# Optimization experiments

Hardware: AMD Instinct MI355X
Metric: run time of the kernel (lower is better)

## Reference

```python
import jax, jax.numpy as jnp
import numpy as np
from jax import lax

UP = 2          # upsampling factor
K = 3           # conv kernel size
PADDING = K // 2
CLAMP = 256.0   # conv_clamp
ACT_GAIN = float(np.sqrt(2.0))  # lrelu def_gain
LRELU_SLOPE = 0.2
_F1 = np.array([1.0, 3.0, 3.0, 1.0], np.float32)
_F1 = _F1 / _F1.sum()  # upfirdn2d.setup_filter normalizes to sum 1


def setup_inputs() -> dict:
    key = jax.random.key(0)
    k1, k2 = jax.random.split(key)
    x = jax.random.normal(k1, (8, 512, 64, 64), jnp.float32)
    weight = jax.random.normal(k2, (256, 512, K, K), jnp.float32)
    bias = jnp.zeros((256,), jnp.float32)
    return {"x": x, "weight": weight, "bias": bias}


def reference(x, weight, bias):
    O, I, kh, kw = weight.shape
    w = weight * (1.0 / np.sqrt(I * kh * kw))  # weight_gain

    # --- conv2d_resample fast path for up=2, kernel>1 ---
    # base padding px0=px1=py0=py1=PADDING, then up>1 adjustments
    fw = _F1.shape[0]
    p0 = PADDING + (fw + UP - 1) // 2
    p1 = PADDING + (fw - UP) // 2
    p0 -= kw - 1
    p1 -= kw - UP
    pt = max(min(-p0, -p1), 0)
    # torch.conv_transpose2d(x, w.transpose(0,1), stride=UP, padding=pt), no weight flip
    # == input-dilated convolution with spatially flipped kernel, pad (k-1-pt)
    y = lax.conv_general_dilated(
        x, jnp.flip(w, (2, 3)),
        window_strides=(1, 1),
        padding=[(kh - 1 - pt, kh - 1 - pt), (kw - 1 - pt, kw - 1 - pt)],
        lhs_dilation=(UP, UP),
        dimension_numbers=('NCHW', 'OIHW', 'NCHW'))  # [N, O, 2H+k-2, 2W+k-2]

    # upfirdn2d: pad (p0+pt, p1+pt) per side, depthwise FIR, gain = up**2
    f2 = jnp.asarray(np.outer(_F1, _F1) * (UP ** 2), jnp.float32)  # [4,4], symmetric
    fk = jnp.broadcast_to(f2[None, None], (O, 1, fw, fw))
    pad = (p0 + pt, p1 + pt)
    y = lax.conv_general_dilated(
        y, fk, (1, 1), padding=[pad, pad],
        dimension_numbers=('NCHW', 'OIHW', 'NCHW'),
        feature_group_count=O)  # [N, O, 2H, 2W]

    # --- bias_act: bias + lrelu * gain, clamp ---
    y = y + bias[None, :, None, None]
    y = jnp.where(y >= 0, y, LRELU_SLOPE * y) * ACT_GAIN
    y = jnp.clip(y, -CLAMP, CLAMP)
    return y
```

## Files before the change

kernel.cpp:

```cpp
#include <hip/hip_runtime.h>
#include <hip/hip_fp16.h>
#include <cstdint>
#include <cmath>


typedef _Float16 f16;
typedef _Float16 f16x8 __attribute__((ext_vector_type(8)));
typedef _Float16 f16x4 __attribute__((ext_vector_type(4)));
typedef float f32x4 __attribute__((ext_vector_type(4)));

#define GLD16(g, l)                                                            \
  __builtin_amdgcn_global_load_lds(                                            \
      (const __attribute__((address_space(1))) void*)(g),                      \
      (__attribute__((address_space(3))) void*)(l), 16, 0, 0)

static const size_t XP_ELEMS  = (size_t)8 * 66 * 66 * 512;
static const size_t XP_BYTES  = XP_ELEMS * 2;
static const size_t WEFF_ELEMS = (size_t)9 * 1024 * 512;
static const size_t WEFF_BYTES = WEFF_ELEMS * 2;

__global__ __launch_bounds__(256) void pad_transpose(const float* __restrict__ x,
                                                     f16* __restrict__ xp) {
  __shared__ f16 tile[64][68];
  const int b = blockIdx.x;
  const int n = b >> 6, h = b & 63, y = h + 1;
  const int t = threadIdx.x;
  for (int c0 = 0; c0 < 512; c0 += 64) {
    if (c0) __syncthreads();
#pragma unroll
    for (int r = 0; r < 16; ++r) {
      int idx = r * 256 + t;
      int cl = idx >> 6, wpos = idx & 63;
      float v = x[(((size_t)(n * 512 + c0 + cl) * 64 + h) << 6) + wpos];
      tile[wpos][cl] = (f16)v;
    }
    __syncthreads();
#pragma unroll
    for (int q = 0; q < 4; ++q) {
      int st = q * 256 + t;
      int xw = st >> 4, c = (st & 15) << 2;
      f16x4 v = *(const f16x4*)&tile[xw][c];
      *(f16x4*)&xp[((size_t)((n * 66 + y) * 66 + xw + 1) << 9) + c0 + c] = v;
    }
  }
}

__global__ __launch_bounds__(256) void weff_kernel(const float* __restrict__ w,
                                                   f16* __restrict__ weff) {
  const int g = blockIdx.x * 256 + threadIdx.x;
  const int o = g >> 9, c = g & 511;
  const float* wp = w + (size_t)(o * 512 + c) * 9;
  float w9[9];
#pragma unroll
  for (int k = 0; k < 9; ++k) w9[k] = wp[k];
  const float f0 = 0.25f, f1 = 0.75f, f2 = 0.75f, f3 = 0.25f;
  const float G[2][3][3] = {
      {{0.f, f0, f1}, {f1, f2, f3}, {f3, 0.f, 0.f}},
      {{0.f, 0.f, f0}, {f0, f1, f2}, {f2, f3, 0.f}}};
  const float scale = 64.f / sqrtf(512.f * 9.f);
#pragma unroll
  for (int py = 0; py < 2; ++py)
#pragma unroll
    for (int dy = 0; dy < 3; ++dy) {
      float ty[3];
#pragma unroll
      for (int bx = 0; bx < 3; ++bx)
        ty[bx] = w9[bx] * G[py][dy][0] + w9[3 + bx] * G[py][dy][1] +
                 w9[6 + bx] * G[py][dy][2];
#pragma unroll
      for (int px = 0; px < 2; ++px)
#pragma unroll
        for (int dx = 0; dx < 3; ++dx) {
          float v = ty[0] * G[px][dx][0] + ty[1] * G[px][dx][1] +
                    ty[2] * G[px][dx][2];
          int s = dy * 3 + dx;
          int col = (o << 2) | (py << 1) | px;
          weff[((size_t)(s * 1024 + col) << 9) + c] = (f16)(v * scale);
        }
    }
}

__global__ __launch_bounds__(256) void conv_main(const f16* __restrict__ xp,
                                                 const f16* __restrict__ weff,
                                                 const float* __restrict__ bias,
                                                 float* __restrict__ out) {
  __shared__ f16 ldsA[128 * 64];
  __shared__ f16 ldsB[128 * 64];
  const int t = threadIdx.x;
  const int lane = t & 63;
  const int wave = t >> 6;
  const int ntile = blockIdx.x;
  const int mtile = blockIdx.y;
  const int n_img = mtile >> 5;
  const int i0 = (mtile & 31) << 1;
  const int col0 = ntile << 7;

  const int c_swz = ((t & 7) ^ ((t >> 3) & 7)) << 3;
  const f16* srcA[4];
  const f16* srcB[4];
#pragma unroll
  for (int q = 0; q < 4; ++q) {
    int pix = (t >> 3) + (q << 5);
    int il = pix >> 6, j = pix & 63;
    srcA[q] = xp + ((size_t)((n_img * 66 + i0 + il) * 66 + j) << 9) + c_swz;
    srcB[q] = weff + ((size_t)(col0 + (t >> 3) + (q << 5)) << 9) + c_swz;
  }
  f16* dstA = ldsA + t * 8;
  f16* dstB = ldsB + t * 8;

  f32x4 acc[4][4];
#pragma unroll
  for (int m = 0; m < 4; ++m)
#pragma unroll
    for (int n = 0; n < 4; ++n) {
      f32x4 z = {0.f, 0.f, 0.f, 0.f};
      acc[m][n] = z;
    }

  const int lrow = lane & 15;
  const int kgrp = lane >> 4;
  const int rA = (wave >> 1) << 6;
  const int cB = (wave & 1) << 6;

  for (int s = 0; s < 9; ++s) {
    const int offA_s = ((s / 3) * 66 + (s % 3)) << 9;
    const int offB_s = s << 19;
    for (int kc = 0; kc < 8; ++kc) {
      const int offA = offA_s + (kc << 6);
      const int offB = offB_s + (kc << 6);
      __syncthreads();
#pragma unroll
      for (int q = 0; q < 4; ++q) GLD16(srcA[q] + offA, dstA + q * 2048);
#pragma unroll
      for (int q = 0; q < 4; ++q) GLD16(srcB[q] + offB, dstB + q * 2048);
      __syncthreads();
#pragma unroll
      for (int kk = 0; kk < 2; ++kk) {
        const int cs = (((kk << 2) | kgrp) ^ (lrow & 7)) << 3;
        f16x8 a[4], b[4];
#pragma unroll
        for (int m = 0; m < 4; ++m)
          a[m] = *(const f16x8*)&ldsA[((rA + (m << 4) + lrow) << 6) + cs];
#pragma unroll
        for (int n = 0; n < 4; ++n)
          b[n] = *(const f16x8*)&ldsB[((cB + (n << 4) + lrow) << 6) + cs];
#pragma unroll
        for (int m = 0; m < 4; ++m)
#pragma unroll
          for (int n = 0; n < 4; ++n)
            acc[m][n] =
                __builtin_amdgcn_mfma_f32_16x16x32_f16(a[m], b[n], acc[m][n], 0, 0, 0);
      }
    }
  }

  const float inv = 1.0f / 64.0f;
#pragma unroll
  for (int nf = 0; nf < 4; ++nf) {
    const int colL = cB + (nf << 4) + lrow;
    const int oG = (col0 + colL) >> 2;
    const int py = (colL >> 1) & 1, px = colL & 1;
    const float bz = bias[oG];
#pragma unroll
    for (int m = 0; m < 4; ++m) {
#pragma unroll
      for (int r = 0; r < 4; ++r) {
        const int rowL = rA + (m << 4) + (kgrp << 2) + r;
        const int ii = i0 + (rowL >> 6), jj = rowL & 63;
        float v = acc[m][nf][r] * inv + bz;
        v = (v < 0.f ? 0.2f * v : v) * 1.41421356237f;
        v = fminf(fmaxf(v, -256.f), 256.f);
        out[((size_t)((n_img * 256 + oG) * 128 + (ii << 1) + py) << 7) +
            (jj << 1) + px] = v;
      }
    }
  }
}

__global__ void naive_conv(const float* __restrict__ x, const float* __restrict__ w,
                           const float* __restrict__ bias, float* __restrict__ out) {
  size_t g = (size_t)blockIdx.x * 256 + threadIdx.x;
  const int xo = g & 127, yo = (int)((g >> 7) & 127);
  const int o = (int)((g >> 14) & 255), n = (int)(g >> 22);
  const int px = xo & 1, py = yo & 1, j = xo >> 1, i = yo >> 1;
  const float f0 = 0.25f, f1 = 0.75f, f2 = 0.75f, f3 = 0.25f;
  const float G0[3][3] = {{0.f, f0, f1}, {f1, f2, f3}, {f3, 0.f, 0.f}};
  const float G1[3][3] = {{0.f, 0.f, f0}, {f0, f1, f2}, {f2, f3, 0.f}};
  const float(*Gy)[3] = py ? G1 : G0;
  const float(*Gx)[3] = px ? G1 : G0;
  float acc = 0.f;
  for (int c = 0; c < 512; ++c) {
    const float* wp = w + ((size_t)o * 512 + c) * 9;
    float w9[9];
#pragma unroll
    for (int k = 0; k < 9; ++k) w9[k] = wp[k];
    float ty[3][3];
#pragma unroll
    for (int dy = 0; dy < 3; ++dy)
#pragma unroll
      for (int bx = 0; bx < 3; ++bx)
        ty[dy][bx] = w9[bx] * Gy[dy][0] + w9[3 + bx] * Gy[dy][1] + w9[6 + bx] * Gy[dy][2];
#pragma unroll
    for (int dy = 0; dy < 3; ++dy) {
      int yy = i + dy - 1;
      if (yy < 0 || yy > 63) continue;
#pragma unroll
      for (int dx = 0; dx < 3; ++dx) {
        int xx = j + dx - 1;
        if (xx < 0 || xx > 63) continue;
        float eff = ty[dy][0] * Gx[dx][0] + ty[dy][1] * Gx[dx][1] + ty[dy][2] * Gx[dx][2];
        acc += x[(((size_t)(n * 512 + c) * 64 + yy) << 6) + xx] * eff;
      }
    }
  }
  float v = acc * (1.f / sqrtf(512.f * 9.f)) + bias[o];
  v = (v < 0.f ? 0.2f * v : v) * 1.41421356237f;
  v = fminf(fmaxf(v, -256.f), 256.f);
  out[g] = v;
}

extern "C" void kernel_launch(void* const* d_in, const int* in_sizes, int n_in,
                              void* d_out, int out_size, void* d_ws, size_t ws_size,
                              hipStream_t stream) {
  const float* x = (const float*)d_in[0];
  const float* w = (const float*)d_in[1];
  const float* bias = (const float*)d_in[2];
  float* out = (float*)d_out;

  const size_t NEED = XP_BYTES + WEFF_BYTES;
  if (ws_size < NEED) {
    naive_conv<<<131072, 256, 0, stream>>>(x, w, bias, out);
    return;
  }
  f16* xp = (f16*)d_ws;
  f16* weff = (f16*)((char*)d_ws + XP_BYTES);

  hipMemsetAsync(d_ws, 0, XP_BYTES, stream);
  pad_transpose<<<512, 256, 0, stream>>>(x, xp);
  weff_kernel<<<512, 256, 0, stream>>>(w, weff);
  conv_main<<<dim3(8, 256), 256, 0, stream>>>(xp, weff, bias, out);
}
```

Before: 553.2 us.

## Rewrite conv GEMM as 256x256 double-buffered pipelined tile with XCD-aware mapping

The main implicit-GEMM kernel moves from a 128x128 tile with 256 threads and single-buffered LDS to a 256x256 tile with 512 threads. LDS is double-buffered and loads are interleaved with MFMA quarter-steps under explicit vmcnt waits, barriers and setprio. Blocks are remapped so tiles that share data land on the same XCD. The full memset of the padded input is replaced by a kernel that zeroes only the border ring, and pad_transpose now runs as more blocks with wider 16-byte stores. The larger tile raises register and LDS pressure, and the hand-tuned barrier schedule is fragile.

```diff
diff --git a/kernel.cpp b/kernel.cpp
--- a/kernel.cpp
+++ b/kernel.cpp
@@ -6,7 +6,6 @@
 
 typedef _Float16 f16;
 typedef _Float16 f16x8 __attribute__((ext_vector_type(8)));
-typedef _Float16 f16x4 __attribute__((ext_vector_type(4)));
 typedef float f32x4 __attribute__((ext_vector_type(4)));
 
 #define GLD16(g, l)                                                            \
@@ -14,34 +13,58 @@
       (const __attribute__((address_space(1))) void*)(g),                      \
       (__attribute__((address_space(3))) void*)(l), 16, 0, 0)
 
-static const size_t XP_ELEMS  = (size_t)8 * 66 * 66 * 512;
-static const size_t XP_BYTES  = XP_ELEMS * 2;
+#define BAR()                                                                  \
+  {                                                                            \
+    __asm__ volatile("" ::: "memory");                                         \
+    __builtin_amdgcn_s_barrier();                                              \
+    __asm__ volatile("" ::: "memory");                                         \
+  }
+#define VMCNT(n) __asm__ volatile("s_waitcnt vmcnt(" #n ")" ::: "memory")
+
+static const size_t XP_ELEMS = (size_t)8 * 66 * 66 * 512;
+static const size_t XP_BYTES = XP_ELEMS * 2;
 static const size_t WEFF_ELEMS = (size_t)9 * 1024 * 512;
 static const size_t WEFF_BYTES = WEFF_ELEMS * 2;
 
+__global__ __launch_bounds__(256) void ring_zero(f16* __restrict__ xp) {
+  int g = blockIdx.x * 256 + threadIdx.x;
+  int n = g / 16640, r = g % 16640;
+  int seg = r >> 6, c8 = r & 63;
+  int y, xc;
+  if (seg < 66) {
+    y = 0; xc = seg;
+  } else if (seg < 132) {
+    y = 65; xc = seg - 66;
+  } else {
+    int rem = seg - 132;
+    y = 1 + (rem >> 1);
+    xc = (rem & 1) * 65;
+  }
+  f16x8 z = {0, 0, 0, 0, 0, 0, 0, 0};
+  *(f16x8*)&xp[((size_t)((n * 66 + y) * 66 + xc) << 9) + (c8 << 3)] = z;
+}
+
 __global__ __launch_bounds__(256) void pad_transpose(const float* __restrict__ x,
                                                      f16* __restrict__ xp) {
-  __shared__ f16 tile[64][68];
+  __shared__ f16 tile[64][132];
   const int b = blockIdx.x;
-  const int n = b >> 6, h = b & 63, y = h + 1;
+  const int cq = b & 3, h = (b >> 2) & 63, n = b >> 8;
   const int t = threadIdx.x;
-  for (int c0 = 0; c0 < 512; c0 += 64) {
-    if (c0) __syncthreads();
-#pragma unroll
-    for (int r = 0; r < 16; ++r) {
-      int idx = r * 256 + t;
-      int cl = idx >> 6, wpos = idx & 63;
-      float v = x[(((size_t)(n * 512 + c0 + cl) * 64 + h) << 6) + wpos];
-      tile[wpos][cl] = (f16)v;
-    }
-    __syncthreads();
-#pragma unroll
-    for (int q = 0; q < 4; ++q) {
-      int st = q * 256 + t;
-      int xw = st >> 4, c = (st & 15) << 2;
-      f16x4 v = *(const f16x4*)&tile[xw][c];
-      *(f16x4*)&xp[((size_t)((n * 66 + y) * 66 + xw + 1) << 9) + c0 + c] = v;
-    }
+  const int c0 = cq << 7;
+#pragma unroll
+  for (int r = 0; r < 32; ++r) {
+    int idx = r * 256 + t;
+    int cl = idx >> 6, w = idx & 63;
+    float v = x[(((size_t)(n * 512 + c0 + cl) * 64 + h) << 6) + w];
+    tile[w][cl] = (f16)v;
+  }
+  __syncthreads();
+#pragma unroll
+  for (int q = 0; q < 4; ++q) {
+    int ch = q * 256 + t;
+    int w = ch >> 4, cc = ch & 15;
+    f16x8 v = *(const f16x8*)&tile[w][cc << 3];
+    *(f16x8*)&xp[((size_t)((n * 66 + h + 1) * 66 + w + 1) << 9) + c0 + (cc << 3)] = v;
   }
 }
 
@@ -80,101 +103,191 @@
     }
 }
 
-__global__ __launch_bounds__(256) void conv_main(const f16* __restrict__ xp,
-                                                 const f16* __restrict__ weff,
-                                                 const float* __restrict__ bias,
-                                                 float* __restrict__ out) {
-  __shared__ f16 ldsA[128 * 64];
-  __shared__ f16 ldsB[128 * 64];
+__global__ __launch_bounds__(512, 2) void conv_main(const f16* __restrict__ xp,
+                                                    const f16* __restrict__ weff,
+                                                    const float* __restrict__ bias,
+                                                    float* __restrict__ out) {
+  __shared__ f16 lds[65536];
+  f16* A0 = lds;
+  f16* A1 = lds + 16384;
+  f16* B0 = lds + 32768;
+  f16* B1 = lds + 49152;
+
   const int t = threadIdx.x;
-  const int lane = t & 63;
-  const int wave = t >> 6;
-  const int ntile = blockIdx.x;
-  const int mtile = blockIdx.y;
-  const int n_img = mtile >> 5;
-  const int i0 = (mtile & 31) << 1;
-  const int col0 = ntile << 7;
+  const int lane = t & 63, wave = t >> 6;
+  const int wm = wave >> 2, wn = wave & 3;
+  const int lrow = lane & 15, kgrp = lane >> 4;
+
+  const int d = blockIdx.x;
+  const int xcd = d & 7, idx = d >> 3;
+  const int ntile = xcd >> 1;
+  const int mtile = ((xcd & 1) << 6) + idx;
+  const int n_img = mtile >> 4;
+  const int i0 = (mtile & 15) << 2;
+  const int col0 = ntile << 8;
 
   const int c_swz = ((t & 7) ^ ((t >> 3) & 7)) << 3;
-  const f16* srcA[4];
-  const f16* srcB[4];
-#pragma unroll
-  for (int q = 0; q < 4; ++q) {
-    int pix = (t >> 3) + (q << 5);
-    int il = pix >> 6, j = pix & 63;
-    srcA[q] = xp + ((size_t)((n_img * 66 + i0 + il) * 66 + j) << 9) + c_swz;
-    srcB[q] = weff + ((size_t)(col0 + (t >> 3) + (q << 5)) << 9) + c_swz;
-  }
-  f16* dstA = ldsA + t * 8;
-  f16* dstB = ldsB + t * 8;
-
-  f32x4 acc[4][4];
-#pragma unroll
-  for (int m = 0; m < 4; ++m)
+  const int jj = t >> 3;
+  const f16* sA[2][2];
+  const f16* sB[2][2];
+#pragma unroll
+  for (int q = 0; q < 2; ++q)
+#pragma unroll
+    for (int h = 0; h < 2; ++h) {
+      sA[q][h] = xp + ((size_t)((n_img * 66 + i0 + h * 2 + q) * 66 + jj) << 9) + c_swz;
+      sB[q][h] = weff + ((size_t)(col0 + h * 128 + q * 64 + jj) << 9) + c_swz;
+    }
+
+#define ST_A(buf, h, off)                                     \
+  {                                                           \
+    GLD16(sA[0][h] + (off), (buf) + (h)*8192 + t * 8);        \
+    GLD16(sA[1][h] + (off), (buf) + (h)*8192 + 4096 + t * 8); \
+  }
+#define ST_B(buf, h, off)                                     \
+  {                                                           \
+    GLD16(sB[0][h] + (off), (buf) + (h)*8192 + t * 8);        \
+    GLD16(sB[1][h] + (off), (buf) + (h)*8192 + 4096 + t * 8); \
+  }
+
+#define OFFS(tt, oa, ob)                                   \
+  {                                                        \
+    int s_ = (tt) >> 3, kc_ = (tt)&7;                      \
+    int dy_ = s_ / 3, dx_ = s_ - 3 * dy_;                  \
+    oa = ((dy_ * 66 + dx_) << 9) + (kc_ << 6);             \
+    ob = (s_ << 19) + (kc_ << 6);                          \
+  }
+
+  f16x8 af[4][2];
+  f16x8 bf[2][2][2];
+  f32x4 acc[8][4];
+#pragma unroll
+  for (int m = 0; m < 8; ++m)
 #pragma unroll
     for (int n = 0; n < 4; ++n) {
       f32x4 z = {0.f, 0.f, 0.f, 0.f};
       acc[m][n] = z;
     }
 
-  const int lrow = lane & 15;
-  const int kgrp = lane >> 4;
-  const int rA = (wave >> 1) << 6;
-  const int cB = (wave & 1) << 6;
-
-  for (int s = 0; s < 9; ++s) {
-    const int offA_s = ((s / 3) * 66 + (s % 3)) << 9;
-    const int offB_s = s << 19;
-    for (int kc = 0; kc < 8; ++kc) {
-      const int offA = offA_s + (kc << 6);
-      const int offB = offB_s + (kc << 6);
-      __syncthreads();
-#pragma unroll
-      for (int q = 0; q < 4; ++q) GLD16(srcA[q] + offA, dstA + q * 2048);
-#pragma unroll
-      for (int q = 0; q < 4; ++q) GLD16(srcB[q] + offB, dstB + q * 2048);
-      __syncthreads();
-#pragma unroll
-      for (int kk = 0; kk < 2; ++kk) {
-        const int cs = (((kk << 2) | kgrp) ^ (lrow & 7)) << 3;
-        f16x8 a[4], b[4];
-#pragma unroll
-        for (int m = 0; m < 4; ++m)
-          a[m] = *(const f16x8*)&ldsA[((rA + (m << 4) + lrow) << 6) + cs];
-#pragma unroll
-        for (int n = 0; n < 4; ++n)
-          b[n] = *(const f16x8*)&ldsB[((cB + (n << 4) + lrow) << 6) + cs];
-#pragma unroll
-        for (int m = 0; m < 4; ++m)
-#pragma unroll
-          for (int n = 0; n < 4; ++n)
-            acc[m][n] =
-                __builtin_amdgcn_mfma_f32_16x16x32_f16(a[m], b[n], acc[m][n], 0, 0, 0);
-      }
-    }
-  }
+#define LDA(bufp, mh)                                                          \
+  _Pragma("unroll") for (int m = 0; m < 4; ++m) _Pragma("unroll") for (int kk = 0; kk < 2; ++kk) \
+      af[m][kk] = *(const f16x8*)&(                                            \
+          bufp)[((wm * 128 + (mh)*64 + m * 16 + lrow) << 6) +                  \
+                ((((kk << 2) | kgrp) ^ (lrow & 7)) << 3)];
+
+#define LDB(bufp, nh)                                                          \
+  _Pragma("unroll") for (int n = 0; n < 2; ++n) _Pragma("unroll") for (int kk = 0; kk < 2; ++kk) \
+      bf[nh][n][kk] = *(const f16x8*)&(                                        \
+          bufp)[((wn * 64 + (nh)*32 + n * 16 + lrow) << 6) +                   \
+                ((((kk << 2) | kgrp) ^ (lrow & 7)) << 3)];
+
+#define MM(mh, nh)                                                             \
+  __builtin_amdgcn_s_setprio(1);                                               \
+  _Pragma("unroll") for (int kk = 0; kk < 2; ++kk)                             \
+  _Pragma("unroll") for (int m = 0; m < 4; ++m)                                \
+  _Pragma("unroll") for (int n = 0; n < 2; ++n)                                \
+      acc[(mh)*4 + m][(nh)*2 + n] = __builtin_amdgcn_mfma_f32_16x16x32_f16(    \
+          af[m][kk], bf[nh][n][kk], acc[(mh)*4 + m][(nh)*2 + n], 0, 0, 0);     \
+  __builtin_amdgcn_s_setprio(0);
+
+  {
+    int oa0, ob0, oa1, ob1;
+    OFFS(0, oa0, ob0);
+    OFFS(1, oa1, ob1);
+    ST_A(A0, 0, oa0);
+    ST_A(A0, 1, oa0);
+    ST_B(B0, 0, ob0);
+    ST_B(B0, 1, ob0);
+    ST_A(A1, 0, oa1);
+    (void)ob1;
+  }
+  VMCNT(2);
+  BAR();
+
+  for (int j = 0; j < 36; ++j) {
+    const int t1 = 2 * j + 1;
+    int tn0 = t1 + 1;
+    if (tn0 > 71) tn0 = 71;
+    int tn1 = t1 + 2;
+    if (tn1 > 71) tn1 = 71;
+    int oa1, ob1, oan0, obn0, oan1, obn1;
+    OFFS(t1, oa1, ob1);
+    OFFS(tn0, oan0, obn0);
+    OFFS(tn1, oan1, obn1);
+    (void)obn1;
+
+    LDA(A0, 0);
+    LDB(B0, 0);
+    ST_A(A1, 1, oa1);
+    BAR();
+    MM(0, 0);
+    BAR();
+    LDB(B0, 1);
+    ST_B(B1, 0, ob1);
+    BAR();
+    MM(0, 1);
+    BAR();
+    LDA(A0, 1);
+    ST_B(B1, 1, ob1);
+    BAR();
+    MM(1, 1);
+    BAR();
+    ST_A(A0, 0, oan0);
+    VMCNT(2);
+    BAR();
+    MM(1, 0);
+    BAR();
+    LDA(A1, 0);
+    LDB(B1, 0);
+    ST_A(A0, 1, oan0);
+    BAR();
+    MM(0, 0);
+    BAR();
+    LDB(B1, 1);
+    ST_B(B0, 0, obn0);
+    BAR();
+    MM(0, 1);
+    BAR();
+    LDA(A1, 1);
+    ST_B(B0, 1, obn0);
+    BAR();
+    MM(1, 1);
+    BAR();
+    ST_A(A1, 0, oan1);
+    VMCNT(2);
+    BAR();
+    MM(1, 0);
+    BAR();
+  }
+  VMCNT(0);
 
   const float inv = 1.0f / 64.0f;
 #pragma unroll
-  for (int nf = 0; nf < 4; ++nf) {
-    const int colL = cB + (nf << 4) + lrow;
-    const int oG = (col0 + colL) >> 2;
-    const int py = (colL >> 1) & 1, px = colL & 1;
+  for (int na = 0; na < 4; ++na) {
+    const int colL = wn * 64 + na * 16 + lrow;
+    const int col = col0 + colL;
+    const int oG = col >> 2;
+    const int py = (col >> 1) & 1, px = col & 1;
     const float bz = bias[oG];
 #pragma unroll
-    for (int m = 0; m < 4; ++m) {
+    for (int ma = 0; ma < 8; ++ma) {
 #pragma unroll
       for (int r = 0; r < 4; ++r) {
-        const int rowL = rA + (m << 4) + (kgrp << 2) + r;
-        const int ii = i0 + (rowL >> 6), jj = rowL & 63;
-        float v = acc[m][nf][r] * inv + bz;
+        const int rowL = wm * 128 + ma * 16 + (kgrp << 2) + r;
+        const int ii = i0 + (rowL >> 6), j2 = rowL & 63;
+        float v = acc[ma][na][r] * inv + bz;
         v = (v < 0.f ? 0.2f * v : v) * 1.41421356237f;
         v = fminf(fmaxf(v, -256.f), 256.f);
         out[((size_t)((n_img * 256 + oG) * 128 + (ii << 1) + py) << 7) +
-            (jj << 1) + px] = v;
+            (j2 << 1) + px] = v;
       }
     }
   }
+#undef ST_A
+#undef ST_B
+#undef OFFS
+#undef LDA
+#undef LDB
+#undef MM
 }
 
 __global__ void naive_conv(const float* __restrict__ x, const float* __restrict__ w,
@@ -199,7 +312,8 @@
     for (int dy = 0; dy < 3; ++dy)
 #pragma unroll
       for (int bx = 0; bx < 3; ++bx)
-        ty[dy][bx] = w9[bx] * Gy[dy][0] + w9[3 + bx] * Gy[dy][1] + w9[6 + bx] * Gy[dy][2];
+        ty[dy][bx] =
+            w9[bx] * Gy[dy][0] + w9[3 + bx] * Gy[dy][1] + w9[6 + bx] * Gy[dy][2];
 #pragma unroll
     for (int dy = 0; dy < 3; ++dy) {
       int yy = i + dy - 1;
@@ -208,7 +322,8 @@
       for (int dx = 0; dx < 3; ++dx) {
         int xx = j + dx - 1;
         if (xx < 0 || xx > 63) continue;
-        float eff = ty[dy][0] * Gx[dx][0] + ty[dy][1] * Gx[dx][1] + ty[dy][2] * Gx[dx][2];
+        float eff =
+            ty[dy][0] * Gx[dx][0] + ty[dy][1] * Gx[dx][1] + ty[dy][2] * Gx[dx][2];
         acc += x[(((size_t)(n * 512 + c) * 64 + yy) << 6) + xx] * eff;
       }
     }
@@ -235,8 +350,8 @@
   f16* xp = (f16*)d_ws;
   f16* weff = (f16*)((char*)d_ws + XP_BYTES);
 
-  hipMemsetAsync(d_ws, 0, XP_BYTES, stream);
-  pad_transpose<<<512, 256, 0, stream>>>(x, xp);
+  ring_zero<<<520, 256, 0, stream>>>(xp);
+  pad_transpose<<<2048, 256, 0, stream>>>(x, xp);
   weff_kernel<<<512, 256, 0, stream>>>(w, weff);
-  conv_main<<<dim3(8, 256), 256, 0, stream>>>(xp, weff, bias, out);
-}
+  conv_main<<<512, 512, 0, stream>>>(xp, weff, bias, out);
+}
```

Result: faster. 477.7 us (-13.6%).
